# Kernel optimization log

Measured on AMD Instinct MI355X. Metric: run time of the kernel, lower is better.

Reference implementation:

```python
import jax, jax.numpy as jnp
import numpy as np

E = 256      # embed_dim
H = 4        # num_heads
EXP = 4      # expansion_factor
B, C, R = 8, 32, 255  # batch, max_cols, rows (seq = R+1 with CLS)
LN_EPS = 1e-5


def setup_inputs() -> dict:
    key = jax.random.key(0)
    ks = jax.random.split(key, 16)
    s = 0.02
    return {
        "x": jax.random.normal(ks[0], (B, C, R, E), jnp.float32),
        "real_cols": jax.random.randint(ks[1], (B,), 0, C + 1),
        "real_rows": jax.random.randint(ks[2], (B,), 0, R + 1),
        "cls_token": jax.random.normal(ks[3], (E,), jnp.float32) * s,
        # MHA in_proj (torch packs q,k,v as (3E, E)) and out_proj
        "w_qkv": jax.random.normal(ks[4], (3 * E, E), jnp.float32) * s,
        "b_qkv": jnp.zeros((3 * E,), jnp.float32),
        "w_out": jax.random.normal(ks[5], (E, E), jnp.float32) * s,
        "b_out": jnp.zeros((E,), jnp.float32),
        # LayerNorm
        "ln_g": jnp.ones((E,), jnp.float32),
        "ln_b": jnp.zeros((E,), jnp.float32),
        # FFN: Linear(E, 4E) -> ReLU -> Linear(4E, E)
        "w1": jax.random.normal(ks[6], (EXP * E, E), jnp.float32) * s,
        "b1": jnp.zeros((EXP * E,), jnp.float32),
        "w2": jax.random.normal(ks[7], (E, EXP * E), jnp.float32) * s,
        "b2": jnp.zeros((E,), jnp.float32),
    }


def reference(x, real_cols, real_rows, cls_token, w_qkv, b_qkv, w_out, b_out,
              ln_g, ln_b, w1, b1, w2, b2):
    Bn, Cn, Rn, En = x.shape
    S = Rn + 1
    Dh = En // H
    dt = x.dtype

    # prepend CLS token to every column's row sequence -> (B, C, S, E)
    cls = jnp.broadcast_to(cls_token.astype(dt), (Bn, Cn, 1, En))
    xc = jnp.concatenate([cls, x], axis=2)

    # fused qkv projection
    qkv = jnp.einsum('bcse,fe->bcsf', xc, w_qkv.astype(dt)) + b_qkv.astype(dt)
    q, k, v = jnp.split(qkv, 3, axis=-1)
    q = q.reshape(Bn, Cn, S, H, Dh)
    k = k.reshape(Bn, Cn, S, H, Dh)
    v = v.reshape(Bn, Cn, S, H, Dh)

    scale = 1.0 / np.sqrt(Dh).astype(np.float32)
    scores = jnp.einsum('bcqhd,bckhd->bchqk', q, k) * scale  # (B,C,H,S,S)

    # key_padding_mask: position 0 (CLS) always valid; row p (1..R) valid iff p <= nrow
    pos = jnp.arange(S)
    valid = (pos[None, :] == 0) | (pos[None, :] <= real_rows[:, None])  # (B, S)
    neg = jnp.asarray(-1e9, scores.dtype)
    scores = jnp.where(valid[:, None, None, None, :], scores, neg)

    attn = jax.nn.softmax(scores, axis=-1)
    ctx = jnp.einsum('bchqk,bckhd->bcqhd', attn, v).reshape(Bn, Cn, S, En)
    mha = jnp.einsum('bcse,fe->bcsf', ctx, w_out.astype(dt)) + b_out.astype(dt)

    # LayerNorm over E
    mu = mha.mean(axis=-1, keepdims=True)
    var = ((mha - mu) ** 2).mean(axis=-1, keepdims=True)
    ln = (mha - mu) * jax.lax.rsqrt(var + LN_EPS) * ln_g.astype(dt) + ln_b.astype(dt)

    # FFN with residual from ln (out = ln + ffn(ln))
    h = jax.nn.relu(jnp.einsum('bcse,fe->bcsf', ln, w1.astype(dt)) + b1.astype(dt))
    ffn = jnp.einsum('bcsf,ef->bcse', h, w2.astype(dt)) + b2.astype(dt)
    out = ln + ffn

    # rep_mode == 'cls': take CLS position; zero out padded columns
    rep = out[:, :, 0, :]  # (B, C, E)
    col_valid = (jnp.arange(Cn)[None, :] < real_cols[:, None]).astype(dt)
    return rep * col_valid[..., None]
```

## Files before the change

kernel.cpp:

```cpp
#include <hip/hip_runtime.h>
#include <hip/hip_bf16.h>
#include <math.h>

static constexpr int kC = 32, kR = 255, kE = 256;

__device__ float g_q0kv[768];
__device__ float g_qw[4 * 256];
__device__ float g_s0[4];
__device__ float g_qb[4];
__device__ float g_m[256 * 4 * 4];
__device__ float g_l[256 * 4 * 4];
__device__ float g_part[256 * 4 * 4 * 256];
__device__ float g_ln[256 * 256];
__device__ float g_hact[256 * 1024];
__device__ unsigned short g_wv_bf[256 * 256];
__device__ unsigned short g_wout_bf[256 * 256];
__device__ unsigned short g_w1_bf[1024 * 256];
__device__ unsigned short g_w2_bf[256 * 1024];

__device__ inline unsigned short f2bf(float f) {
  __hip_bfloat16 h = __float2bfloat16(f);
  return __builtin_bit_cast(unsigned short, h);
}
__device__ inline float bflo(unsigned int u) { return __uint_as_float(u << 16); }
__device__ inline float bfhi(unsigned int u) { return __uint_as_float(u & 0xffff0000u); }

__global__ __launch_bounds__(256) void k_setup_rows(const float* __restrict__ cls,
                                                    const float* __restrict__ w_qkv,
                                                    const float* __restrict__ b_qkv) {
  const int t = threadIdx.x, wv = t >> 6, l = t & 63;
  const int row = blockIdx.x * 4 + wv;
  float4 w4 = *((const float4*)(w_qkv + (size_t)row * 256) + l);
  float4 c4 = *((const float4*)cls + l);
  float a = w4.x * c4.x + w4.y * c4.y + w4.z * c4.z + w4.w * c4.w;
#pragma unroll
  for (int m = 1; m < 64; m <<= 1) a += __shfl_xor(a, m);
  if (l == 0) g_q0kv[row] = a + b_qkv[row];
}

__global__ __launch_bounds__(256) void k_setup_head(const float* __restrict__ w_qkv,
                                                    const float* __restrict__ b_qkv,
                                                    const float* __restrict__ w_out,
                                                    const float* __restrict__ w1,
                                                    const float* __restrict__ w2) {
  const int t = threadIdx.x, wvi = t >> 6, l = t & 63;
  if (blockIdx.x >= 4) {
    const int u = blockIdx.x - 4;
    const float* src;
    unsigned short* dst;
    int R, C, o0, e0;
    if (u < 4) { src = w_qkv + 512 * 256; dst = g_wv_bf; R = 256; C = 256; o0 = u * 64; e0 = 0; }
    else if (u < 8) { src = w_out; dst = g_wout_bf; R = 256; C = 256; o0 = (u - 4) * 64; e0 = 0; }
    else if (u < 24) { src = w1; dst = g_w1_bf; R = 1024; C = 256; o0 = (u - 8) * 64; e0 = 0; }
    else { const int v = u - 24; src = w2; dst = g_w2_bf; R = 256; C = 1024; o0 = (v >> 2) * 64; e0 = (v & 3) * 256; }

    __shared__ unsigned short tile[64 * 260];
    for (int r = wvi; r < 64; r += 4) {
      float4 v = *((const float4*)(src + (size_t)(o0 + r) * C + e0) + l);
      ushort4 ov;
      ov.x = f2bf(v.x); ov.y = f2bf(v.y); ov.z = f2bf(v.z); ov.w = f2bf(v.w);
      *(ushort4*)&tile[r * 260 + 4 * l] = ov;
    }
    __syncthreads();
    const int e80 = e0 >> 3;
    for (int e8l = wvi; e8l < 32; e8l += 4) {
      const unsigned int* tp = (const unsigned int*)&tile[l * 260 + e8l * 8];
      uint4 o;
      o.x = tp[0]; o.y = tp[1]; o.z = tp[2]; o.w = tp[3];
      *(uint4*)(dst + ((size_t)(e80 + e8l) * R + o0 + l) * 8) = o;
    }
    return;
  }

  const int h = blockIdx.x;
  __shared__ float q0h[64];
  if (t < 64) q0h[t] = g_q0kv[h * 64 + t];
  __syncthreads();
  float acc = 0.f;
#pragma unroll 8
  for (int j = 0; j < 64; ++j)
    acc += q0h[j] * w_qkv[(size_t)(256 + h * 64 + j) * 256 + t];
  g_qw[h * 256 + t] = acc * 0.125f;
  if (wvi == 0) {
    const float q = q0h[l];
    float pk = q * g_q0kv[256 + h * 64 + l];
    float pb = q * b_qkv[256 + h * 64 + l];
#pragma unroll
    for (int m = 1; m < 64; m <<= 1) {
      pk += __shfl_xor(pk, m);
      pb += __shfl_xor(pb, m);
    }
    if (l == 0) {
      g_s0[h] = pk * 0.125f;
      g_qb[h] = pb * 0.125f;
    }
  }
}

__global__ __launch_bounds__(256) void k_attn(const float* __restrict__ x,
                                              const int* __restrict__ real_cols,
                                              const int* __restrict__ real_rows) {
  const int bc = blockIdx.x, chunk = blockIdx.y;
  const int b = bc >> 5, c = bc & 31;
  if (c >= real_cols[b]) return;
  const int rr = real_rows[b];
  const int r0 = chunk * 64;
  const int nr = min(64, rr - r0);
  if (nr <= 0) return;

  __shared__ float xs[64][260];
  __shared__ float qws[4][256];
  __shared__ float ps[4][64];
  const int t = threadIdx.x, wv = t >> 6, l = t & 63;

#pragma unroll
  for (int i = 0; i < 4; ++i) qws[i][t] = g_qw[i * 256 + t];

  const float* xb = x + ((size_t)bc * kR + r0) * kE;
  for (int r = wv; r < nr; r += 4)
    *(float4*)&xs[r][4 * l] = *(const float4*)(xb + (size_t)r * kE + 4 * l);
  __syncthreads();

  const int h = wv, row = l;
  float acc = 0.f;
  const float4* qrow = (const float4*)&qws[h][0];
  const float4* xrow = (const float4*)&xs[row][0];
#pragma unroll 8
  for (int e4 = 0; e4 < 64; ++e4) {
    float4 q4 = qrow[e4];
    float4 x4 = xrow[e4];
    acc += q4.x * x4.x + q4.y * x4.y + q4.z * x4.z + q4.w * x4.w;
  }
  float s = (row < nr) ? acc + g_qb[h] : -1e30f;
  float mx = s;
#pragma unroll
  for (int m = 1; m < 64; m <<= 1) mx = fmaxf(mx, __shfl_xor(mx, m));
  float p = (row < nr) ? __expf(s - mx) : 0.f;
  float lsum = p;
#pragma unroll
  for (int m = 1; m < 64; m <<= 1) lsum += __shfl_xor(lsum, m);
  ps[h][row] = p;
  if (l == 0) {
    g_m[(bc * 4 + chunk) * 4 + h] = mx;
    g_l[(bc * 4 + chunk) * 4 + h] = lsum;
  }
  __syncthreads();

  float a0 = 0.f, a1 = 0.f, a2 = 0.f, a3 = 0.f;
  for (int r2 = 0; r2 < nr; ++r2) {
    float xv = xs[r2][t];
    a0 += ps[0][r2] * xv;
    a1 += ps[1][r2] * xv;
    a2 += ps[2][r2] * xv;
    a3 += ps[3][r2] * xv;
  }
  float* pp = g_part + (size_t)(bc * 4 + chunk) * 4 * 256;
  pp[0 * 256 + t] = a0;
  pp[1 * 256 + t] = a1;
  pp[2 * 256 + t] = a2;
  pp[3 * 256 + t] = a3;
}

__global__ __launch_bounds__(256) void k_tail(const int* __restrict__ real_cols,
                                              const int* __restrict__ real_rows,
                                              const float* __restrict__ b_qkv,
                                              const float* __restrict__ b_out,
                                              const float* __restrict__ ln_g,
                                              const float* __restrict__ ln_b) {
  const int bc = blockIdx.x, b = bc >> 5, c = bc & 31;
  if (c >= real_cols[b]) return;
  const int rr = real_rows[b];
  const int nch = (rr + 63) >> 6;
  const int t = threadIdx.x, wv = t >> 6, l = t & 63;

  __shared__ float xb[4][256];
  __shared__ float ctxs[256];
  __shared__ float al[4][4];
  __shared__ float p0s[4];
  __shared__ float rb[2][4];

  if (t < 4) {
    const int h = t;
    const float s0 = g_s0[h];
    float M = s0;
    for (int ch = 0; ch < nch; ++ch) M = fmaxf(M, g_m[(bc * 4 + ch) * 4 + h]);
    float lt = __expf(s0 - M);
    const float w0 = lt;
    float av[4] = {0.f, 0.f, 0.f, 0.f};
    for (int ch = 0; ch < nch; ++ch) {
      float e = __expf(g_m[(bc * 4 + ch) * 4 + h] - M);
      av[ch] = e;
      lt += g_l[(bc * 4 + ch) * 4 + h] * e;
    }
    const float inv = 1.f / lt;
#pragma unroll
    for (int ch = 0; ch < 4; ++ch) al[h][ch] = av[ch] * inv;
    p0s[h] = w0 * inv;
  }
  __syncthreads();

#pragma unroll
  for (int h = 0; h < 4; ++h) {
    float a = 0.f;
    for (int ch = 0; ch < nch; ++ch)
      a += al[h][ch] * g_part[(size_t)(bc * 4 + ch) * 4 * 256 + h * 256 + t];
    xb[h][t] = a;
  }
  __syncthreads();

  {
    const int h = wv;
    const float p0 = p0s[h];
    float acc = p0 * g_q0kv[512 + t] + (1.f - p0) * b_qkv[512 + t];
    const uint4* wr = (const uint4*)g_wv_bf;
    const float4* v4p = (const float4*)&xb[h][0];
#pragma unroll 4
    for (int e8 = 0; e8 < 32; ++e8) {
      uint4 w = wr[e8 * 256 + t];
      float4 a = v4p[2 * e8], bb = v4p[2 * e8 + 1];
      acc += bflo(w.x) * a.x + bfhi(w.x) * a.y + bflo(w.y) * a.z + bfhi(w.y) * a.w +
             bflo(w.z) * bb.x + bfhi(w.z) * bb.y + bflo(w.w) * bb.z + bfhi(w.w) * bb.w;
    }
    ctxs[t] = acc;
  }
  __syncthreads();

  float mh;
  {
    float acc = b_out[t];
    const uint4* wr = (const uint4*)g_wout_bf;
    const float4* c4 = (const float4*)&ctxs[0];
#pragma unroll 4
    for (int e8 = 0; e8 < 32; ++e8) {
      uint4 w = wr[e8 * 256 + t];
      float4 a = c4[2 * e8], bb = c4[2 * e8 + 1];
      acc += bflo(w.x) * a.x + bfhi(w.x) * a.y + bflo(w.y) * a.z + bfhi(w.y) * a.w +
             bflo(w.z) * bb.x + bfhi(w.z) * bb.y + bflo(w.w) * bb.z + bfhi(w.w) * bb.w;
    }
    mh = acc;
  }

  float s1 = mh, s2 = mh * mh;
#pragma unroll
  for (int m = 1; m < 64; m <<= 1) {
    s1 += __shfl_xor(s1, m);
    s2 += __shfl_xor(s2, m);
  }
  if (l == 0) {
    rb[0][wv] = s1;
    rb[1][wv] = s2;
  }
  __syncthreads();
  const float mu = (rb[0][0] + rb[0][1] + rb[0][2] + rb[0][3]) * (1.f / 256.f);
  const float msq = (rb[1][0] + rb[1][1] + rb[1][2] + rb[1][3]) * (1.f / 256.f);
  const float var = msq - mu * mu;
  g_ln[(size_t)bc * 256 + t] =
      (mh - mu) * rsqrtf(var + 1e-5f) * ln_g[t] + ln_b[t];
}

__global__ __launch_bounds__(256) void k_ffn1(const float* __restrict__ b1,
                                              const int* __restrict__ real_cols) {
  const int tok0 = blockIdx.x * 8;
  const int b = tok0 >> 5, c0 = tok0 & 31;
  if (c0 >= real_cols[b]) return;
  __shared__ float lns[8][256];
  const int t = threadIdx.x;
  const int f0 = blockIdx.y * 128;
#pragma unroll
  for (int i = 0; i < 8; ++i) lns[i][t] = g_ln[(size_t)(tok0 + i) * 256 + t];
  __syncthreads();
  const int f = f0 + (t & 127), half = t >> 7;
  const uint4* wr = (const uint4*)g_w1_bf;
  const float bb = b1[f];
  float acc[4] = {bb, bb, bb, bb};
  for (int e8 = 0; e8 < 32; ++e8) {
    uint4 w = wr[e8 * 1024 + f];
    const float w0 = bflo(w.x), w1v = bfhi(w.x), w2v = bflo(w.y), w3 = bfhi(w.y);
    const float w4v = bflo(w.z), w5 = bfhi(w.z), w6 = bflo(w.w), w7 = bfhi(w.w);
#pragma unroll
    for (int k = 0; k < 4; ++k) {
      const int i = half * 4 + k;
      const float4 a = *(const float4*)&lns[i][8 * e8];
      const float4 bbv = *(const float4*)&lns[i][8 * e8 + 4];
      acc[k] += w0 * a.x + w1v * a.y + w2v * a.z + w3 * a.w +
                w4v * bbv.x + w5 * bbv.y + w6 * bbv.z + w7 * bbv.w;
    }
  }
#pragma unroll
  for (int k = 0; k < 4; ++k)
    g_hact[(size_t)(tok0 + half * 4 + k) * 1024 + f] = fmaxf(acc[k], 0.f);
}

__global__ __launch_bounds__(256) void k_ffn2(const float* __restrict__ b2,
                                              const int* __restrict__ real_cols,
                                              float* __restrict__ out) {
  const int t = threadIdx.x;
  const int tok0 = blockIdx.x * 8, e0 = blockIdx.y * 32;
  const int b = tok0 >> 5, c0 = tok0 & 31;
  const int ncols = real_cols[b];
  if (c0 >= ncols) {
    out[(size_t)(tok0 + (t >> 5)) * 256 + e0 + (t & 31)] = 0.f;
    return;
  }
  __shared__ float hs[8][1024];
#pragma unroll
  for (int i = 0; i < 8; ++i) {
#pragma unroll
    for (int j = 0; j < 4; ++j)
      hs[i][j * 256 + t] = g_hact[(size_t)(tok0 + i) * 1024 + j * 256 + t];
  }
  __syncthreads();
  const int e = e0 + (t & 31), i = t >> 5;
  const int tok = tok0 + i, c = tok & 31;
  const uint4* wr = (const uint4*)g_w2_bf;
  const float4* h4 = (const float4*)&hs[i][0];
  float acc = b2[e];
  for (int f8 = 0; f8 < 128; ++f8) {
    uint4 w = wr[f8 * 256 + e];
    float4 a = h4[2 * f8], bb = h4[2 * f8 + 1];
    acc += bflo(w.x) * a.x + bfhi(w.x) * a.y + bflo(w.y) * a.z + bfhi(w.y) * a.w +
           bflo(w.z) * bb.x + bfhi(w.z) * bb.y + bflo(w.w) * bb.z + bfhi(w.w) * bb.w;
  }
  const float lnv = g_ln[(size_t)tok * 256 + e];
  out[(size_t)tok * 256 + e] = (c < ncols) ? (lnv + acc) : 0.f;
}

extern "C" void kernel_launch(void* const* d_in, const int* in_sizes, int n_in,
                              void* d_out, int out_size, void* d_ws, size_t ws_size,
                              hipStream_t stream) {
  const float* x = (const float*)d_in[0];
  const int* real_cols = (const int*)d_in[1];
  const int* real_rows = (const int*)d_in[2];
  const float* cls = (const float*)d_in[3];
  const float* w_qkv = (const float*)d_in[4];
  const float* b_qkv = (const float*)d_in[5];
  const float* w_out = (const float*)d_in[6];
  const float* b_out = (const float*)d_in[7];
  const float* ln_g = (const float*)d_in[8];
  const float* ln_b = (const float*)d_in[9];
  const float* w1 = (const float*)d_in[10];
  const float* b1 = (const float*)d_in[11];
  const float* w2 = (const float*)d_in[12];
  const float* b2 = (const float*)d_in[13];
  float* out = (float*)d_out;
  (void)in_sizes; (void)n_in; (void)out_size; (void)d_ws; (void)ws_size;

  k_setup_rows<<<192, 256, 0, stream>>>(cls, w_qkv, b_qkv);
  k_setup_head<<<44, 256, 0, stream>>>(w_qkv, b_qkv, w_out, w1, w2);
  k_attn<<<dim3(256, 4), 256, 0, stream>>>(x, real_cols, real_rows);
  k_tail<<<256, 256, 0, stream>>>(real_cols, real_rows, b_qkv, b_out, ln_g, ln_b);
  k_ffn1<<<dim3(32, 8), 256, 0, stream>>>(b1, real_cols);
  k_ffn2<<<dim3(32, 8), 256, 0, stream>>>(b2, real_cols, out);
}
```

Before: 179.0 us.

## Fuse setup kernels and merge tail, FFN1, FFN2 into one per-token kernel

The two setup kernels become one. Head blocks now compute their own q0 and k-cls rows directly instead of waiting on a prior kernel, and the remaining blocks compute only the V rows. The tail, FFN1 and FFN2 kernels are merged into a single per-token kernel that keeps the LayerNorm output and hidden activations in shared memory. This cuts three kernel launches and the global round trips through g_ln and g_hact. In exchange, each token block streams the full bf16 W1/W2 weights alone instead of sharing them across 8 tokens, so L2 weight traffic rises and parallelism drops to 256 blocks.

```diff
diff --git a/kernel.cpp b/kernel.cpp
--- a/kernel.cpp
+++ b/kernel.cpp
@@ -11,8 +11,6 @@
 __device__ float g_m[256 * 4 * 4];
 __device__ float g_l[256 * 4 * 4];
 __device__ float g_part[256 * 4 * 4 * 256];
-__device__ float g_ln[256 * 256];
-__device__ float g_hact[256 * 1024];
 __device__ unsigned short g_wv_bf[256 * 256];
 __device__ unsigned short g_wout_bf[256 * 256];
 __device__ unsigned short g_w1_bf[1024 * 256];
@@ -25,25 +23,25 @@
 __device__ inline float bflo(unsigned int u) { return __uint_as_float(u << 16); }
 __device__ inline float bfhi(unsigned int u) { return __uint_as_float(u & 0xffff0000u); }
 
-__global__ __launch_bounds__(256) void k_setup_rows(const float* __restrict__ cls,
-                                                    const float* __restrict__ w_qkv,
-                                                    const float* __restrict__ b_qkv) {
-  const int t = threadIdx.x, wv = t >> 6, l = t & 63;
-  const int row = blockIdx.x * 4 + wv;
-  float4 w4 = *((const float4*)(w_qkv + (size_t)row * 256) + l);
-  float4 c4 = *((const float4*)cls + l);
-  float a = w4.x * c4.x + w4.y * c4.y + w4.z * c4.z + w4.w * c4.w;
-#pragma unroll
-  for (int m = 1; m < 64; m <<= 1) a += __shfl_xor(a, m);
-  if (l == 0) g_q0kv[row] = a + b_qkv[row];
-}
-
-__global__ __launch_bounds__(256) void k_setup_head(const float* __restrict__ w_qkv,
-                                                    const float* __restrict__ b_qkv,
-                                                    const float* __restrict__ w_out,
-                                                    const float* __restrict__ w1,
-                                                    const float* __restrict__ w2) {
+__global__ __launch_bounds__(256) void k_setup(const float* __restrict__ cls,
+                                               const float* __restrict__ w_qkv,
+                                               const float* __restrict__ b_qkv,
+                                               const float* __restrict__ w_out,
+                                               const float* __restrict__ w1,
+                                               const float* __restrict__ w2) {
   const int t = threadIdx.x, wvi = t >> 6, l = t & 63;
+
+  if (blockIdx.x >= 44) {
+    const int row = 512 + (blockIdx.x - 44) * 4 + wvi;
+    float4 w4 = *((const float4*)(w_qkv + (size_t)row * 256) + l);
+    float4 c4 = *((const float4*)cls + l);
+    float a = w4.x * c4.x + w4.y * c4.y + w4.z * c4.z + w4.w * c4.w;
+#pragma unroll
+    for (int m = 1; m < 64; m <<= 1) a += __shfl_xor(a, m);
+    if (l == 0) g_q0kv[row] = a + b_qkv[row];
+    return;
+  }
+
   if (blockIdx.x >= 4) {
     const int u = blockIdx.x - 4;
     const float* src;
@@ -74,8 +72,27 @@
 
   const int h = blockIdx.x;
   __shared__ float q0h[64];
-  if (t < 64) q0h[t] = g_q0kv[h * 64 + t];
-  __syncthreads();
+  __shared__ float kch[64];
+  {
+    const int r = t >> 1, half = t & 1;
+    const int row = (r < 64) ? (h * 64 + r) : (256 + h * 64 + (r - 64));
+    const float4* wp = (const float4*)(w_qkv + (size_t)row * 256 + half * 128);
+    const float4* cp = (const float4*)cls + half * 32;
+    float a = 0.f;
+#pragma unroll 8
+    for (int j = 0; j < 32; ++j) {
+      float4 w4 = wp[j];
+      float4 cv = cp[j];
+      a += w4.x * cv.x + w4.y * cv.y + w4.z * cv.z + w4.w * cv.w;
+    }
+    a += __shfl_xor(a, 1);
+    if (half == 0) {
+      const float val = a + b_qkv[row];
+      if (r < 64) q0h[r] = val; else kch[r - 64] = val;
+    }
+  }
+  __syncthreads();
+
   float acc = 0.f;
 #pragma unroll 8
   for (int j = 0; j < 64; ++j)
@@ -83,7 +100,7 @@
   g_qw[h * 256 + t] = acc * 0.125f;
   if (wvi == 0) {
     const float q = q0h[l];
-    float pk = q * g_q0kv[256 + h * 64 + l];
+    float pk = q * kch[l];
     float pb = q * b_qkv[256 + h * 64 + l];
 #pragma unroll
     for (int m = 1; m < 64; m <<= 1) {
@@ -161,20 +178,28 @@
   pp[3 * 256 + t] = a3;
 }
 
-__global__ __launch_bounds__(256) void k_tail(const int* __restrict__ real_cols,
-                                              const int* __restrict__ real_rows,
-                                              const float* __restrict__ b_qkv,
-                                              const float* __restrict__ b_out,
-                                              const float* __restrict__ ln_g,
-                                              const float* __restrict__ ln_b) {
+__global__ __launch_bounds__(256) void k_token(const int* __restrict__ real_cols,
+                                               const int* __restrict__ real_rows,
+                                               const float* __restrict__ b_qkv,
+                                               const float* __restrict__ b_out,
+                                               const float* __restrict__ ln_g,
+                                               const float* __restrict__ ln_b,
+                                               const float* __restrict__ b1,
+                                               const float* __restrict__ b2,
+                                               float* __restrict__ out) {
   const int bc = blockIdx.x, b = bc >> 5, c = bc & 31;
-  if (c >= real_cols[b]) return;
+  const int t = threadIdx.x, wv = t >> 6, l = t & 63;
+  if (c >= real_cols[b]) {
+    out[(size_t)bc * 256 + t] = 0.f;
+    return;
+  }
   const int rr = real_rows[b];
   const int nch = (rr + 63) >> 6;
-  const int t = threadIdx.x, wv = t >> 6, l = t & 63;
 
   __shared__ float xb[4][256];
   __shared__ float ctxs[256];
+  __shared__ float lns[256];
+  __shared__ float hs[1024];
   __shared__ float al[4][4];
   __shared__ float p0s[4];
   __shared__ float rb[2][4];
@@ -254,75 +279,42 @@
   const float mu = (rb[0][0] + rb[0][1] + rb[0][2] + rb[0][3]) * (1.f / 256.f);
   const float msq = (rb[1][0] + rb[1][1] + rb[1][2] + rb[1][3]) * (1.f / 256.f);
   const float var = msq - mu * mu;
-  g_ln[(size_t)bc * 256 + t] =
-      (mh - mu) * rsqrtf(var + 1e-5f) * ln_g[t] + ln_b[t];
-}
-
-__global__ __launch_bounds__(256) void k_ffn1(const float* __restrict__ b1,
-                                              const int* __restrict__ real_cols) {
-  const int tok0 = blockIdx.x * 8;
-  const int b = tok0 >> 5, c0 = tok0 & 31;
-  if (c0 >= real_cols[b]) return;
-  __shared__ float lns[8][256];
-  const int t = threadIdx.x;
-  const int f0 = blockIdx.y * 128;
-#pragma unroll
-  for (int i = 0; i < 8; ++i) lns[i][t] = g_ln[(size_t)(tok0 + i) * 256 + t];
-  __syncthreads();
-  const int f = f0 + (t & 127), half = t >> 7;
-  const uint4* wr = (const uint4*)g_w1_bf;
-  const float bb = b1[f];
-  float acc[4] = {bb, bb, bb, bb};
-  for (int e8 = 0; e8 < 32; ++e8) {
-    uint4 w = wr[e8 * 1024 + f];
-    const float w0 = bflo(w.x), w1v = bfhi(w.x), w2v = bflo(w.y), w3 = bfhi(w.y);
-    const float w4v = bflo(w.z), w5 = bfhi(w.z), w6 = bflo(w.w), w7 = bfhi(w.w);
-#pragma unroll
-    for (int k = 0; k < 4; ++k) {
-      const int i = half * 4 + k;
-      const float4 a = *(const float4*)&lns[i][8 * e8];
-      const float4 bbv = *(const float4*)&lns[i][8 * e8 + 4];
-      acc[k] += w0 * a.x + w1v * a.y + w2v * a.z + w3 * a.w +
-                w4v * bbv.x + w5 * bbv.y + w6 * bbv.z + w7 * bbv.w;
-    }
-  }
-#pragma unroll
-  for (int k = 0; k < 4; ++k)
-    g_hact[(size_t)(tok0 + half * 4 + k) * 1024 + f] = fmaxf(acc[k], 0.f);
-}
-
-__global__ __launch_bounds__(256) void k_ffn2(const float* __restrict__ b2,
-                                              const int* __restrict__ real_cols,
-                                              float* __restrict__ out) {
-  const int t = threadIdx.x;
-  const int tok0 = blockIdx.x * 8, e0 = blockIdx.y * 32;
-  const int b = tok0 >> 5, c0 = tok0 & 31;
-  const int ncols = real_cols[b];
-  if (c0 >= ncols) {
-    out[(size_t)(tok0 + (t >> 5)) * 256 + e0 + (t & 31)] = 0.f;
-    return;
-  }
-  __shared__ float hs[8][1024];
-#pragma unroll
-  for (int i = 0; i < 8; ++i) {
-#pragma unroll
-    for (int j = 0; j < 4; ++j)
-      hs[i][j * 256 + t] = g_hact[(size_t)(tok0 + i) * 1024 + j * 256 + t];
-  }
-  __syncthreads();
-  const int e = e0 + (t & 31), i = t >> 5;
-  const int tok = tok0 + i, c = tok & 31;
-  const uint4* wr = (const uint4*)g_w2_bf;
-  const float4* h4 = (const float4*)&hs[i][0];
-  float acc = b2[e];
-  for (int f8 = 0; f8 < 128; ++f8) {
-    uint4 w = wr[f8 * 256 + e];
-    float4 a = h4[2 * f8], bb = h4[2 * f8 + 1];
-    acc += bflo(w.x) * a.x + bfhi(w.x) * a.y + bflo(w.y) * a.z + bfhi(w.y) * a.w +
-           bflo(w.z) * bb.x + bfhi(w.z) * bb.y + bflo(w.w) * bb.z + bfhi(w.w) * bb.w;
-  }
-  const float lnv = g_ln[(size_t)tok * 256 + e];
-  out[(size_t)tok * 256 + e] = (c < ncols) ? (lnv + acc) : 0.f;
+  const float lnv = (mh - mu) * rsqrtf(var + 1e-5f) * ln_g[t] + ln_b[t];
+  lns[t] = lnv;
+  __syncthreads();
+
+  {
+    const uint4* wr = (const uint4*)g_w1_bf;
+    float acc1[4];
+#pragma unroll
+    for (int k = 0; k < 4; ++k) acc1[k] = b1[t + 256 * k];
+    for (int e8 = 0; e8 < 32; ++e8) {
+      const float4 a = *(const float4*)&lns[8 * e8];
+      const float4 bbv = *(const float4*)&lns[8 * e8 + 4];
+#pragma unroll
+      for (int k = 0; k < 4; ++k) {
+        uint4 w = wr[e8 * 1024 + t + 256 * k];
+        acc1[k] += bflo(w.x) * a.x + bfhi(w.x) * a.y + bflo(w.y) * a.z + bfhi(w.y) * a.w +
+                   bflo(w.z) * bbv.x + bfhi(w.z) * bbv.y + bflo(w.w) * bbv.z + bfhi(w.w) * bbv.w;
+      }
+    }
+#pragma unroll
+    for (int k = 0; k < 4; ++k) hs[t + 256 * k] = fmaxf(acc1[k], 0.f);
+  }
+  __syncthreads();
+
+  {
+    const uint4* wr = (const uint4*)g_w2_bf;
+    const float4* h4 = (const float4*)&hs[0];
+    float acc = b2[t];
+    for (int f8 = 0; f8 < 128; ++f8) {
+      uint4 w = wr[f8 * 256 + t];
+      float4 a = h4[2 * f8], bb = h4[2 * f8 + 1];
+      acc += bflo(w.x) * a.x + bfhi(w.x) * a.y + bflo(w.y) * a.z + bfhi(w.y) * a.w +
+             bflo(w.z) * bb.x + bfhi(w.z) * bb.y + bflo(w.w) * bb.z + bfhi(w.w) * bb.w;
+    }
+    out[(size_t)bc * 256 + t] = lnv + acc;
+  }
 }
 
 extern "C" void kernel_launch(void* const* d_in, const int* in_sizes, int n_in,
@@ -345,10 +337,7 @@
   float* out = (float*)d_out;
   (void)in_sizes; (void)n_in; (void)out_size; (void)d_ws; (void)ws_size;
 
-  k_setup_rows<<<192, 256, 0, stream>>>(cls, w_qkv, b_qkv);
-  k_setup_head<<<44, 256, 0, stream>>>(w_qkv, b_qkv, w_out, w1, w2);
+  k_setup<<<108, 256, 0, stream>>>(cls, w_qkv, b_qkv, w_out, w1, w2);
   k_attn<<<dim3(256, 4), 256, 0, stream>>>(x, real_cols, real_rows);
-  k_tail<<<256, 256, 0, stream>>>(real_cols, real_rows, b_qkv, b_out, ln_g, ln_b);
-  k_ffn1<<<dim3(32, 8), 256, 0, stream>>>(b1, real_cols);
-  k_ffn2<<<dim3(32, 8), 256, 0, stream>>>(b2, real_cols, out);
-}
+  k_token<<<256, 256, 0, stream>>>(real_cols, real_rows, b_qkv, b_out, ln_g, ln_b, b1, b2, out);
+}
```

After: 177.7 us. No clear change (-0.8%).
